# Performance work log

Measured on AMD Instinct MI355X. Metric: run time of the kernel, lower is better.

Reference implementation:

```python
import jax, jax.numpy as jnp
import numpy as np

D_MODEL = 512
N_HEADS = 8
D_K = D_MODEL // N_HEADS  # 64
MAX_LEN = 5000


def _positional_encoding(d_model, max_len):
    pe = np.zeros((max_len, d_model), dtype=np.float32)
    position = np.arange(max_len, dtype=np.float32)[:, None]
    div_term = np.exp(np.arange(0, d_model, 2, dtype=np.float32) * (-np.log(10000.0) / d_model))
    pe[:, 0::2] = np.sin(position * div_term)
    pe[:, 1::2] = np.cos(position * div_term)
    return jnp.asarray(pe)


def _layer_norm(x, gamma, beta, eps):
    mu = jnp.mean(x, axis=-1, keepdims=True)
    var = jnp.mean(jnp.square(x - mu), axis=-1, keepdims=True)
    return (x - mu) * jax.lax.rsqrt(var + eps) * gamma + beta


def setup_inputs() -> dict:
    key = jax.random.key(0)
    ks = jax.random.split(key, 5)
    s = 1.0 / np.sqrt(D_MODEL)
    return {
        "x": jax.random.normal(ks[0], (4, 2048, D_MODEL), dtype=jnp.float32),
        "ln1_g": jnp.ones((D_MODEL,), jnp.float32),
        "ln1_b": jnp.zeros((D_MODEL,), jnp.float32),
        "wq": jax.random.normal(ks[1], (D_MODEL, D_MODEL), jnp.float32) * s,
        "wk": jax.random.normal(ks[2], (D_MODEL, D_MODEL), jnp.float32) * s,
        "wv": jax.random.normal(ks[3], (D_MODEL, D_MODEL), jnp.float32) * s,
        "wfc": jax.random.normal(ks[4], (D_MODEL, D_MODEL), jnp.float32) * s,
        "ln2_g": jnp.ones((D_MODEL,), jnp.float32),
        "ln2_b": jnp.zeros((D_MODEL,), jnp.float32),
    }


def reference(x, ln1_g, ln1_b, wq, wk, wv, wfc, ln2_g, ln2_b):
    B, T, D = x.shape
    residual0 = x
    # outer pre-norm (nn.LayerNorm default eps=1e-5)
    h = _layer_norm(x, ln1_g, ln1_b, 1e-5)
    # sinusoidal positional encoding
    h = h + _positional_encoding(D_MODEL, MAX_LEN)[:T]
    residual1 = h
    # projections -> [B, H, T, d]
    q = (h @ wq).reshape(B, T, N_HEADS, D_K).transpose(0, 2, 1, 3)
    k = (h @ wk).reshape(B, T, N_HEADS, D_K).transpose(0, 2, 1, 3)
    v = (h @ wv).reshape(B, T, N_HEADS, D_K).transpose(0, 2, 1, 3)
    scale = 1.0 / np.sqrt(D_K).astype(np.float32)
    attn = jnp.einsum("bhqd,bhkd->bhqk", q * scale, k)
    causal = jnp.tril(jnp.ones((T, T), dtype=bool))  # subsequent mask
    attn = jnp.where(causal, attn, jnp.float32(-1e9))
    attn = jax.nn.softmax(attn, axis=-1)
    o = jnp.einsum("bhqk,bhkd->bhqd", attn, v)
    o = o.transpose(0, 2, 1, 3).reshape(B, T, D)
    o = o @ wfc
    # inner post-attention residual + LayerNorm (eps=1e-6)
    h2 = _layer_norm(o + residual1, ln2_g, ln2_b, 1e-6)
    return h2 + residual0
```

## Files before the change

### kernel.cpp

```cpp
#include <hip/hip_runtime.h>
#include <hip/hip_bf16.h>

#define B_ 4
#define T_ 2048
#define D_ 512

typedef __attribute__((ext_vector_type(8))) short short8;
typedef __attribute__((ext_vector_type(4))) short short4v;
typedef __attribute__((ext_vector_type(4))) float float4v;
typedef unsigned short bf16_t;

__device__ __forceinline__ bf16_t f2bf(float f) {
  unsigned int u = __builtin_bit_cast(unsigned int, f);
  unsigned int r = (u + 0x7fffu + ((u >> 16) & 1u)) >> 16;
  return (bf16_t)r;
}
__device__ __forceinline__ float bf2f(bf16_t b) {
  unsigned int u = ((unsigned int)b) << 16;
  return __builtin_bit_cast(float, u);
}

__device__ __forceinline__ float fast_exp2(float x) {
#if __has_builtin(__builtin_amdgcn_exp2f)
  return __builtin_amdgcn_exp2f(x);
#else
  float r;
  asm("v_exp_f32 %0, %1" : "=v"(r) : "v"(x));
  return r;
#endif
}

__device__ __forceinline__ unsigned cvt_pk_bf16(float lo, float hi) {
  unsigned r;
  asm("v_cvt_pk_bf16_f32 %0, %1, %2" : "=v"(r) : "v"(lo), "v"(hi));
  return r;
}

__device__ __forceinline__ float waveReduceSum(float v) {
#pragma unroll
  for (int m = 32; m >= 1; m >>= 1) v += __shfl_xor(v, m, 64);
  return v;
}

__device__ __forceinline__ void gld16(const bf16_t* g, bf16_t* l) {
  __builtin_amdgcn_global_load_lds(
      (const __attribute__((address_space(1))) void*)g,
      (__attribute__((address_space(3))) void*)l, 16, 0, 0);
}

__global__ __launch_bounds__(256) void pre_kernel(
    const float* __restrict__ x, const float* __restrict__ g,
    const float* __restrict__ bb,
    const float* __restrict__ wq, const float* __restrict__ wk,
    const float* __restrict__ wv, const float* __restrict__ wfc,
    bf16_t* __restrict__ h_bf16,
    bf16_t* __restrict__ wqkvT, bf16_t* __restrict__ wfcT) {
  if (blockIdx.x >= 2048) {
    __shared__ float tl[64][65];
    int bid = blockIdx.x - 2048;
    const float* src;
    float scl;
    int n0, k0;
    bf16_t* dst;
    if (bid < 192) {
      n0 = (bid >> 3) * 64;
      k0 = (bid & 7) * 64;
      int m = n0 >> 9;
      src = (m == 0) ? wq : ((m == 1) ? wk : wv);
      scl = (m == 0) ? 1.4426950408889634f : ((m == 1) ? 0.125f : 1.0f);
      dst = wqkvT;
    } else {
      int local = bid - 192;
      n0 = (local >> 3) * 64;
      k0 = (local & 7) * 64;
      src = wfc;
      scl = 1.0f;
      dst = wfcT;
    }
    int c0 = n0 & 511;
    int jl = threadIdx.x & 63, bi = threadIdx.x >> 6;
#pragma unroll
    for (int it = 0; it < 16; ++it) {
      int i = it * 4 + bi;
      tl[jl][i] = src[(size_t)(k0 + i) * 512 + c0 + jl] * scl;
    }
    __syncthreads();
    int i2 = (threadIdx.x & 31) * 2, jb = threadIdx.x >> 5;
#pragma unroll
    for (int it = 0; it < 8; ++it) {
      int j = it * 8 + jb;
      unsigned pk = cvt_pk_bf16(tl[j][i2], tl[j][i2 + 1]);
      *(unsigned*)(dst + (size_t)(n0 + j) * 512 + k0 + i2) = pk;
    }
    return;
  }
  int wave = threadIdx.x >> 6, lane = threadIdx.x & 63;
  int row = blockIdx.x * 4 + wave;
  int pos = row & (T_ - 1);
  const float* xr = x + (size_t)row * D_;
  int c0 = lane * 8;
  float v[8];
  float4 a = *(const float4*)(xr + c0);
  float4 b4 = *(const float4*)(xr + c0 + 4);
  v[0]=a.x; v[1]=a.y; v[2]=a.z; v[3]=a.w;
  v[4]=b4.x; v[5]=b4.y; v[6]=b4.z; v[7]=b4.w;
  float s = 0.f;
#pragma unroll
  for (int j = 0; j < 8; ++j) s += v[j];
  s = waveReduceSum(s);
  float mu = s * (1.f / 512.f);
  float q = 0.f;
#pragma unroll
  for (int j = 0; j < 8; ++j) { float d = v[j] - mu; q += d * d; }
  q = waveReduceSum(q);
  float rstd = rsqrtf(q * (1.f / 512.f) + 1e-5f);
  bf16_t* hb = h_bf16 + (size_t)row * D_;
  float fpos = (float)pos;
#pragma unroll
  for (int jp = 0; jp < 4; ++jp) {
    int col = c0 + jp * 2;
    float dt = fast_exp2((float)col * (-13.287712379549449f / 512.0f));
    float ang = fpos * dt;
    float hn0 = (v[2 * jp] - mu) * rstd * g[col] + bb[col] + __sinf(ang);
    float hn1 = (v[2 * jp + 1] - mu) * rstd * g[col + 1] + bb[col + 1] + __cosf(ang);
    hb[col] = f2bf(hn0);
    hb[col + 1] = f2bf(hn1);
  }
}

template <typename EPI>
__device__ __forceinline__ void gemm_body(const bf16_t* __restrict__ A,
                                          const bf16_t* __restrict__ Bt,
                                          int m0, int n0, bf16_t* As, bf16_t* Bs,
                                          EPI epi) {
  const int tid = threadIdx.x;
  const int w = tid >> 6, lane = tid & 63;
  const int ln = lane & 15, quad = lane >> 4;
  const int wy = w >> 1, wx = w & 1;
  const int sw = ln & 7;

  float4v acc[4][4];
  float4v z = {0.f, 0.f, 0.f, 0.f};
#pragma unroll
  for (int i = 0; i < 4; ++i)
#pragma unroll
    for (int j = 0; j < 4; ++j) acc[i][j] = z;

  for (int k0 = 0; k0 < 512; k0 += 64) {
#pragma unroll
    for (int i = 0; i < 4; ++i) {
      int cbase = w * 256 + i * 64;
      int chunk = cbase + lane;
      int row = chunk >> 3;
      int lb = (chunk & 7) ^ (row & 7);
      gld16(A + (size_t)(m0 + row) * 512 + k0 + lb * 8, As + cbase * 8);
      gld16(Bt + (size_t)(n0 + row) * 512 + k0 + lb * 8, Bs + cbase * 8);
    }
    __syncthreads();
#pragma unroll
    for (int c = 0; c < 2; ++c) {
      short8 af[4], bf[4];
#pragma unroll
      for (int mt = 0; mt < 4; ++mt)
        af[mt] = *(const short8*)(As + (wy * 64 + mt * 16 + ln) * 64 + (((c * 4 + quad) ^ sw)) * 8);
#pragma unroll
      for (int nt = 0; nt < 4; ++nt)
        bf[nt] = *(const short8*)(Bs + (wx * 64 + nt * 16 + ln) * 64 + (((c * 4 + quad) ^ sw)) * 8);
#pragma unroll
      for (int mt = 0; mt < 4; ++mt)
#pragma unroll
        for (int nt = 0; nt < 4; ++nt)
          acc[mt][nt] = __builtin_amdgcn_mfma_f32_16x16x32_bf16(af[mt], bf[nt], acc[mt][nt], 0, 0, 0);
    }
    __syncthreads();
  }
#pragma unroll
  for (int mt = 0; mt < 4; ++mt)
#pragma unroll
    for (int r = 0; r < 4; ++r) {
      int row = m0 + wy * 64 + mt * 16 + quad * 4 + r;
#pragma unroll
      for (int nt = 0; nt < 4; ++nt) {
        int col = n0 + wx * 64 + nt * 16 + ln;
        epi(row, col, acc[mt][nt][r]);
      }
    }
}

template <typename EPI>
__device__ __forceinline__ void gemm_body_64x128(const bf16_t* __restrict__ A,
                                                 const bf16_t* __restrict__ Bt,
                                                 int m0, int n0, bf16_t* As, bf16_t* Bs,
                                                 EPI epi) {
  const int tid = threadIdx.x;
  const int w = tid >> 6, lane = tid & 63;
  const int ln = lane & 15, quad = lane >> 4;
  const int wy = w >> 1, wx = w & 1;
  const int sw = ln & 7;

  float4v acc[2][4];
  float4v z = {0.f, 0.f, 0.f, 0.f};
#pragma unroll
  for (int i = 0; i < 2; ++i)
#pragma unroll
    for (int j = 0; j < 4; ++j) acc[i][j] = z;

  for (int k0 = 0; k0 < 512; k0 += 64) {
#pragma unroll
    for (int i = 0; i < 2; ++i) {
      int cbase = i * 256 + w * 64;
      int chunk = cbase + lane;
      int row = chunk >> 3;
      int lb = (chunk & 7) ^ (row & 7);
      gld16(A + (size_t)(m0 + row) * 512 + k0 + lb * 8, As + cbase * 8);
    }
#pragma unroll
    for (int i = 0; i < 4; ++i) {
      int cbase = i * 256 + w * 64;
      int chunk = cbase + lane;
      int row = chunk >> 3;
      int lb = (chunk & 7) ^ (row & 7);
      gld16(Bt + (size_t)(n0 + row) * 512 + k0 + lb * 8, Bs + cbase * 8);
    }
    __syncthreads();
#pragma unroll
    for (int c = 0; c < 2; ++c) {
      short8 af[2], bf[4];
#pragma unroll
      for (int mt = 0; mt < 2; ++mt)
        af[mt] = *(const short8*)(As + (wy * 32 + mt * 16 + ln) * 64 + (((c * 4 + quad) ^ sw)) * 8);
#pragma unroll
      for (int nt = 0; nt < 4; ++nt)
        bf[nt] = *(const short8*)(Bs + (wx * 64 + nt * 16 + ln) * 64 + (((c * 4 + quad) ^ sw)) * 8);
#pragma unroll
      for (int mt = 0; mt < 2; ++mt)
#pragma unroll
        for (int nt = 0; nt < 4; ++nt)
          acc[mt][nt] = __builtin_amdgcn_mfma_f32_16x16x32_bf16(af[mt], bf[nt], acc[mt][nt], 0, 0, 0);
    }
    __syncthreads();
  }
#pragma unroll
  for (int mt = 0; mt < 2; ++mt)
#pragma unroll
    for (int r = 0; r < 4; ++r) {
      int row = m0 + wy * 32 + mt * 16 + quad * 4 + r;
#pragma unroll
      for (int nt = 0; nt < 4; ++nt) {
        int col = n0 + wx * 64 + nt * 16 + ln;
        epi(row, col, acc[mt][nt][r]);
      }
    }
}

__global__ __launch_bounds__(256) void gemm_qkvt_kernel(
    const bf16_t* __restrict__ h_bf, const bf16_t* __restrict__ wqkvT,
    bf16_t* __restrict__ qk, bf16_t* __restrict__ vT) {
  __shared__ __align__(16) bf16_t As[128 * 64];
  __shared__ __align__(16) bf16_t Bs[128 * 64];
  int bx = blockIdx.x;
  if (bx < 512) {
    int m0 = (bx >> 3) * 128, n0 = (bx & 7) * 128;
    gemm_body(h_bf, wqkvT, m0, n0, As, Bs,
              [&](int row, int col, float v) { qk[(size_t)row * 1024 + col] = f2bf(v); });
  } else {
    int local = bx - 512;
    int m0 = (local >> 6) * 128, n0 = (local & 63) * 128;
    gemm_body(wqkvT + 1024 * 512, h_bf, m0, n0, As, Bs,
              [&](int row, int col, float v) { vT[(size_t)row * 8192 + col] = f2bf(v); });
  }
}

__global__ __launch_bounds__(256) void gemm_out_kernel(
    const bf16_t* __restrict__ attn, const bf16_t* __restrict__ wfcT,
    const bf16_t* __restrict__ h_bf, bf16_t* __restrict__ o2r) {
  __shared__ __align__(16) bf16_t As[64 * 64];
  __shared__ __align__(16) bf16_t Bs[128 * 64];
  int bx = blockIdx.x;
  int m0 = (bx >> 2) * 64, n0 = (bx & 3) * 128;
  gemm_body_64x128(attn, wfcT, m0, n0, As, Bs, [&](int row, int col, float v) {
    size_t o = (size_t)row * 512 + col;
    o2r[o] = f2bf(v + bf2f(h_bf[o]));
  });
}

__global__ __launch_bounds__(256) void attn_kernel(const bf16_t* __restrict__ qk,
                                                   const bf16_t* __restrict__ vT,
                                                   bf16_t* __restrict__ out) {
  __shared__ __align__(16) bf16_t Ks[2][64 * 64];
  __shared__ __align__(16) bf16_t Vs[2][64 * 64];
  const int bx = blockIdx.x;
  const int qt = 31 - (bx >> 5);
  const int bh = bx & 31;
  const int b = bh >> 3, h = bh & 7;
  const int tid = threadIdx.x;
  const int w = tid >> 6, lane = tid & 63;
  const int ln = lane & 15, quad = lane >> 4;
  const int sw = ln & 7;

  short8 qf0, qf1;
  {
    size_t qrow = ((size_t)b * T_ + qt * 64 + w * 16 + ln) * 1024 + h * 64;
    qf0 = *(const short8*)(qk + qrow + quad * 8);
    qf1 = *(const short8*)(qk + qrow + 32 + quad * 8);
  }
  float4v z = {0.f, 0.f, 0.f, 0.f};
  float4v oacc[4];
#pragma unroll
  for (int i = 0; i < 4; ++i) oacc[i] = z;
  float m_s = -1e30f, l_s = 0.f;

  const bf16_t* kbase = qk + (size_t)b * T_ * 1024 + 512 + h * 64;
  const bf16_t* vbase = vT + (size_t)(h * 64) * 8192 + (size_t)b * T_;

  const int cb0 = w * 128, cb1 = w * 128 + 64;
  const int ch0 = cb0 + lane, ch1 = cb1 + lane;
  const int r0 = ch0 >> 3, r1 = ch1 >> 3;
  const int lb0 = (ch0 & 7) ^ (r0 & 7), lb1 = (ch1 & 7) ^ (r1 & 7);
  const bf16_t* kg0 = kbase + (size_t)r0 * 1024 + lb0 * 8;
  const bf16_t* kg1 = kbase + (size_t)r1 * 1024 + lb1 * 8;
  const bf16_t* vg0 = vbase + (size_t)r0 * 8192 + lb0 * 8;
  const bf16_t* vg1 = vbase + (size_t)r1 * 8192 + lb1 * 8;

  auto stage2 = [&](int buf) {
    gld16(kg0, Ks[buf] + cb0 * 8);
    gld16(kg1, Ks[buf] + cb1 * 8);
    gld16(vg0, Vs[buf] + cb0 * 8);
    gld16(vg1, Vs[buf] + cb1 * 8);
    kg0 += 64 * 1024; kg1 += 64 * 1024;
    vg0 += 64;        vg1 += 64;
  };

  auto compute = [&](const bf16_t* Kc, const bf16_t* Vc, bool mask) {
    float sv[4][4];
#pragma unroll
    for (int mt = 0; mt < 4; ++mt) {
      float4v st = z;
      int row = mt * 16 + ln;
      short8 a0 = *(const short8*)(Kc + row * 64 + ((0 + quad) ^ sw) * 8);
      short8 a1 = *(const short8*)(Kc + row * 64 + ((4 + quad) ^ sw) * 8);
      st = __builtin_amdgcn_mfma_f32_16x16x32_bf16(a0, qf0, st, 0, 0, 0);
      st = __builtin_amdgcn_mfma_f32_16x16x32_bf16(a1, qf1, st, 0, 0, 0);
#pragma unroll
      for (int r = 0; r < 4; ++r) {
        float v = st[r];
        if (mask) {
          int kloc = mt * 16 + quad * 4 + r;
          if (kloc > w * 16 + ln) v = -1e30f;
        }
        sv[mt][r] = v;
      }
    }
    float mx = sv[0][0];
#pragma unroll
    for (int mt = 0; mt < 4; ++mt)
#pragma unroll
      for (int r = 0; r < 4; ++r) mx = fmaxf(mx, sv[mt][r]);
    mx = fmaxf(mx, __shfl_xor(mx, 16, 64));
    mx = fmaxf(mx, __shfl_xor(mx, 32, 64));
    if (!__all(mx <= m_s + 8.0f)) {
      float mn = fmaxf(m_s, mx);
      float alpha = fast_exp2(m_s - mn);
      m_s = mn;
      l_s *= alpha;
#pragma unroll
      for (int dt = 0; dt < 4; ++dt)
#pragma unroll
        for (int r = 0; r < 4; ++r) oacc[dt][r] *= alpha;
    }
    float rs = 0.f;
#pragma unroll
    for (int mt = 0; mt < 4; ++mt)
#pragma unroll
      for (int r = 0; r < 4; ++r) {
        float p = fast_exp2(sv[mt][r] - m_s);
        sv[mt][r] = p;
        rs += p;
      }
    rs += __shfl_xor(rs, 16, 64);
    rs += __shfl_xor(rs, 32, 64);
    l_s += rs;
    short4v pf[4];
#pragma unroll
    for (int mt = 0; mt < 4; ++mt) {
      uint2 pp;
      pp.x = cvt_pk_bf16(sv[mt][0], sv[mt][1]);
      pp.y = cvt_pk_bf16(sv[mt][2], sv[mt][3]);
      pf[mt] = __builtin_bit_cast(short4v, pp);
    }
#pragma unroll
    for (int dt = 0; dt < 4; ++dt) {
      int row = dt * 16 + ln;
#pragma unroll
      for (int mt = 0; mt < 4; ++mt) {
        short4v av = *(const short4v*)(Vc + row * 64 + ((2 * mt + (quad >> 1)) ^ sw) * 8 + (quad & 1) * 4);
        oacc[dt] = __builtin_amdgcn_mfma_f32_16x16x16bf16_1k(av, pf[mt], oacc[dt], 0, 0, 0);
      }
    }
  };

  stage2(0);
  __syncthreads();
  for (int kt = 0; kt < qt; ++kt) {
    int cur = kt & 1;
    stage2(cur ^ 1);
    compute(Ks[cur], Vs[cur], false);
    __syncthreads();
  }
  compute(Ks[qt & 1], Vs[qt & 1], true);

  float inv = 1.0f / l_s;
  size_t obase = ((size_t)b * T_ + qt * 64 + w * 16 + ln) * 512 + h * 64;
#pragma unroll
  for (int dt = 0; dt < 4; ++dt) {
    short4v o4;
#pragma unroll
    for (int r = 0; r < 4; ++r) o4[r] = (short)f2bf(oacc[dt][r] * inv);
    *(short4v*)(out + obase + dt * 16 + quad * 4) = o4;
  }
}

__global__ __launch_bounds__(256) void ln2_kernel(
    const bf16_t* __restrict__ o2r, const float* __restrict__ x,
    const float* __restrict__ g, const float* __restrict__ bb,
    float* __restrict__ out) {
  int wave = threadIdx.x >> 6, lane = threadIdx.x & 63;
  int row = blockIdx.x * 4 + wave;
  size_t ro = (size_t)row * D_;
  int c0 = lane * 8;
  short8 ov = *(const short8*)(o2r + ro + c0);
  float t[8];
#pragma unroll
  for (int j = 0; j < 8; ++j) t[j] = bf2f((bf16_t)ov[j]);
  float s = 0.f;
#pragma unroll
  for (int j = 0; j < 8; ++j) s += t[j];
  s = waveReduceSum(s);
  float mu = s * (1.f / 512.f);
  float q = 0.f;
#pragma unroll
  for (int j = 0; j < 8; ++j) { float d = t[j] - mu; q += d * d; }
  q = waveReduceSum(q);
  float rstd = rsqrtf(q * (1.f / 512.f) + 1e-6f);
  float4 x0 = *(const float4*)(x + ro + c0);
  float4 x1 = *(const float4*)(x + ro + c0 + 4);
  float xr[8] = {x0.x, x0.y, x0.z, x0.w, x1.x, x1.y, x1.z, x1.w};
  float o[8];
#pragma unroll
  for (int j = 0; j < 8; ++j) {
    int col = c0 + j;
    o[j] = (t[j] - mu) * rstd * g[col] + bb[col] + xr[j];
  }
  float4 w0 = {o[0], o[1], o[2], o[3]};
  float4 w1 = {o[4], o[5], o[6], o[7]};
  *(float4*)(out + ro + c0) = w0;
  *(float4*)(out + ro + c0 + 4) = w1;
}

extern "C" void kernel_launch(void* const* d_in, const int* in_sizes, int n_in,
                              void* d_out, int out_size, void* d_ws, size_t ws_size,
                              hipStream_t stream) {
  const float* x   = (const float*)d_in[0];
  const float* g1  = (const float*)d_in[1];
  const float* b1  = (const float*)d_in[2];
  const float* wq  = (const float*)d_in[3];
  const float* wk  = (const float*)d_in[4];
  const float* wv  = (const float*)d_in[5];
  const float* wfc = (const float*)d_in[6];
  const float* g2  = (const float*)d_in[7];
  const float* b2  = (const float*)d_in[8];
  float* out = (float*)d_out;

  char* ws = (char*)d_ws;
  const size_t O_HBF  = 0;
  const size_t O_WQKV = 8388608;
  const size_t O_WFC  = 9961472;
  const size_t O_QK   = 10485760;
  const size_t O_VT   = 27262976;
  const size_t O_ATTN = 35651584;
  const size_t O_O2R  = 44040192;
  const size_t WS_NEED = 52428800;
  if (ws_size < WS_NEED) return;

  bf16_t* h_bf  = (bf16_t*)(ws + O_HBF);
  bf16_t* wqkvT = (bf16_t*)(ws + O_WQKV);
  bf16_t* wfcT  = (bf16_t*)(ws + O_WFC);
  bf16_t* qk    = (bf16_t*)(ws + O_QK);
  bf16_t* vT    = (bf16_t*)(ws + O_VT);
  bf16_t* attn  = (bf16_t*)(ws + O_ATTN);
  bf16_t* o2r   = (bf16_t*)(ws + O_O2R);

  pre_kernel<<<dim3(2304), dim3(256), 0, stream>>>(x, g1, b1, wq, wk, wv, wfc,
                                                   h_bf, wqkvT, wfcT);
  gemm_qkvt_kernel<<<dim3(768), dim3(256), 0, stream>>>(h_bf, wqkvT, qk, vT);
  attn_kernel<<<dim3(1024), dim3(256), 0, stream>>>(qk, vT, attn);
  gemm_out_kernel<<<dim3(512), dim3(256), 0, stream>>>(attn, wfcT, h_bf, o2r);
  ln2_kernel<<<dim3(2048), dim3(256), 0, stream>>>(o2r, x, g2, b2, out);
}
```

Baseline: 161.8 us.

## Process two query tiles per attention block to reuse staged K/V tiles

Each attention block now handles 128 query rows (two 64-row sub-tiles) instead of 64, so every K/V tile loaded into shared memory feeds MFMAs for both sub-tiles. The grid is halved to 512 blocks, and the first sub-tile stops early with its own mask on its diagonal tile. This cuts global-to-LDS traffic and sync count per query row, but doubles accumulator registers (lower occupancy) and gives fewer, longer blocks with more uneven causal work.

After: 186.7 us. 1.15x slower.

```diff
diff --git a/kernel.cpp b/kernel.cpp
--- a/kernel.cpp
+++ b/kernel.cpp
@@ -290,7 +290,7 @@
   __shared__ __align__(16) bf16_t Ks[2][64 * 64];
   __shared__ __align__(16) bf16_t Vs[2][64 * 64];
   const int bx = blockIdx.x;
-  const int qt = 31 - (bx >> 5);
+  const int t = 15 - (bx >> 5);
   const int bh = bx & 31;
   const int b = bh >> 3, h = bh & 7;
   const int tid = threadIdx.x;
@@ -298,17 +298,22 @@
   const int ln = lane & 15, quad = lane >> 4;
   const int sw = ln & 7;
 
-  short8 qf0, qf1;
-  {
-    size_t qrow = ((size_t)b * T_ + qt * 64 + w * 16 + ln) * 1024 + h * 64;
-    qf0 = *(const short8*)(qk + qrow + quad * 8);
-    qf1 = *(const short8*)(qk + qrow + 32 + quad * 8);
+  const int Nt = 2 * t + 2;
+
+  short8 qf[2][2];
+#pragma unroll
+  for (int s = 0; s < 2; ++s) {
+    size_t qrow = ((size_t)b * T_ + t * 128 + s * 64 + w * 16 + ln) * 1024 + h * 64;
+    qf[s][0] = *(const short8*)(qk + qrow + quad * 8);
+    qf[s][1] = *(const short8*)(qk + qrow + 32 + quad * 8);
   }
   float4v z = {0.f, 0.f, 0.f, 0.f};
-  float4v oacc[4];
-#pragma unroll
-  for (int i = 0; i < 4; ++i) oacc[i] = z;
-  float m_s = -1e30f, l_s = 0.f;
+  float4v oacc[2][4];
+#pragma unroll
+  for (int s = 0; s < 2; ++s)
+#pragma unroll
+    for (int i = 0; i < 4; ++i) oacc[s][i] = z;
+  float m_s[2] = {-1e30f, -1e30f}, l_s[2] = {0.f, 0.f};
 
   const bf16_t* kbase = qk + (size_t)b * T_ * 1024 + 512 + h * 64;
   const bf16_t* vbase = vT + (size_t)(h * 64) * 8192 + (size_t)b * T_;
@@ -331,56 +336,35 @@
     vg0 += 64;        vg1 += 64;
   };
 
-  auto compute = [&](const bf16_t* Kc, const bf16_t* Vc, bool mask) {
-    float sv[4][4];
-#pragma unroll
-    for (int mt = 0; mt < 4; ++mt) {
-      float4v st = z;
-      int row = mt * 16 + ln;
-      short8 a0 = *(const short8*)(Kc + row * 64 + ((0 + quad) ^ sw) * 8);
-      short8 a1 = *(const short8*)(Kc + row * 64 + ((4 + quad) ^ sw) * 8);
-      st = __builtin_amdgcn_mfma_f32_16x16x32_bf16(a0, qf0, st, 0, 0, 0);
-      st = __builtin_amdgcn_mfma_f32_16x16x32_bf16(a1, qf1, st, 0, 0, 0);
-#pragma unroll
-      for (int r = 0; r < 4; ++r) {
-        float v = st[r];
-        if (mask) {
-          int kloc = mt * 16 + quad * 4 + r;
-          if (kloc > w * 16 + ln) v = -1e30f;
-        }
-        sv[mt][r] = v;
-      }
-    }
-    float mx = sv[0][0];
+  auto softmax = [&](float sv[4][4], float& ms, float& ls, float4v* oa, short4v* pf) {
+    float mxa[4];
 #pragma unroll
     for (int mt = 0; mt < 4; ++mt)
-#pragma unroll
-      for (int r = 0; r < 4; ++r) mx = fmaxf(mx, sv[mt][r]);
+      mxa[mt] = fmaxf(fmaxf(sv[mt][0], sv[mt][1]), fmaxf(sv[mt][2], sv[mt][3]));
+    float mx = fmaxf(fmaxf(mxa[0], mxa[1]), fmaxf(mxa[2], mxa[3]));
     mx = fmaxf(mx, __shfl_xor(mx, 16, 64));
     mx = fmaxf(mx, __shfl_xor(mx, 32, 64));
-    if (!__all(mx <= m_s + 8.0f)) {
-      float mn = fmaxf(m_s, mx);
-      float alpha = fast_exp2(m_s - mn);
-      m_s = mn;
-      l_s *= alpha;
+    if (!__all(mx <= ms + 8.0f)) {
+      float mn = fmaxf(ms, mx);
+      float alpha = fast_exp2(ms - mn);
+      ms = mn;
+      ls *= alpha;
 #pragma unroll
       for (int dt = 0; dt < 4; ++dt)
 #pragma unroll
-        for (int r = 0; r < 4; ++r) oacc[dt][r] *= alpha;
-    }
-    float rs = 0.f;
-#pragma unroll
-    for (int mt = 0; mt < 4; ++mt)
-#pragma unroll
-      for (int r = 0; r < 4; ++r) {
-        float p = fast_exp2(sv[mt][r] - m_s);
-        sv[mt][r] = p;
-        rs += p;
-      }
+        for (int r = 0; r < 4; ++r) oa[dt][r] *= alpha;
+    }
+    float rsa[4];
+#pragma unroll
+    for (int mt = 0; mt < 4; ++mt) {
+#pragma unroll
+      for (int r = 0; r < 4; ++r) sv[mt][r] = fast_exp2(sv[mt][r] - ms);
+      rsa[mt] = (sv[mt][0] + sv[mt][1]) + (sv[mt][2] + sv[mt][3]);
+    }
+    float rs = (rsa[0] + rsa[1]) + (rsa[2] + rsa[3]);
     rs += __shfl_xor(rs, 16, 64);
     rs += __shfl_xor(rs, 32, 64);
-    l_s += rs;
-    short4v pf[4];
+    ls += rs;
 #pragma unroll
     for (int mt = 0; mt < 4; ++mt) {
       uint2 pp;
@@ -388,35 +372,79 @@
       pp.y = cvt_pk_bf16(sv[mt][2], sv[mt][3]);
       pf[mt] = __builtin_bit_cast(short4v, pp);
     }
+  };
+
+  auto compute = [&](const bf16_t* Kc, const bf16_t* Vc,
+                     bool act0, bool mask0, bool mask1) {
+    float sv0[4][4], sv1[4][4];
+#pragma unroll
+    for (int mt = 0; mt < 4; ++mt) {
+      int row = mt * 16 + ln;
+      short8 a0 = *(const short8*)(Kc + row * 64 + ((0 + quad) ^ sw) * 8);
+      short8 a1 = *(const short8*)(Kc + row * 64 + ((4 + quad) ^ sw) * 8);
+      float4v st1 = z;
+      st1 = __builtin_amdgcn_mfma_f32_16x16x32_bf16(a0, qf[1][0], st1, 0, 0, 0);
+      st1 = __builtin_amdgcn_mfma_f32_16x16x32_bf16(a1, qf[1][1], st1, 0, 0, 0);
+      if (act0) {
+        float4v st0 = z;
+        st0 = __builtin_amdgcn_mfma_f32_16x16x32_bf16(a0, qf[0][0], st0, 0, 0, 0);
+        st0 = __builtin_amdgcn_mfma_f32_16x16x32_bf16(a1, qf[0][1], st0, 0, 0, 0);
+#pragma unroll
+        for (int r = 0; r < 4; ++r) {
+          float v = st0[r];
+          if (mask0) {
+            int kloc = mt * 16 + quad * 4 + r;
+            if (kloc > w * 16 + ln) v = -1e30f;
+          }
+          sv0[mt][r] = v;
+        }
+      }
+#pragma unroll
+      for (int r = 0; r < 4; ++r) {
+        float v = st1[r];
+        if (mask1) {
+          int kloc = mt * 16 + quad * 4 + r;
+          if (kloc > w * 16 + ln) v = -1e30f;
+        }
+        sv1[mt][r] = v;
+      }
+    }
+    short4v pf0[4], pf1[4];
+    if (act0) softmax(sv0, m_s[0], l_s[0], oacc[0], pf0);
+    softmax(sv1, m_s[1], l_s[1], oacc[1], pf1);
 #pragma unroll
     for (int dt = 0; dt < 4; ++dt) {
       int row = dt * 16 + ln;
 #pragma unroll
       for (int mt = 0; mt < 4; ++mt) {
         short4v av = *(const short4v*)(Vc + row * 64 + ((2 * mt + (quad >> 1)) ^ sw) * 8 + (quad & 1) * 4);
-        oacc[dt] = __builtin_amdgcn_mfma_f32_16x16x16bf16_1k(av, pf[mt], oacc[dt], 0, 0, 0);
+        if (act0)
+          oacc[0][dt] = __builtin_amdgcn_mfma_f32_16x16x16bf16_1k(av, pf0[mt], oacc[0][dt], 0, 0, 0);
+        oacc[1][dt] = __builtin_amdgcn_mfma_f32_16x16x16bf16_1k(av, pf1[mt], oacc[1][dt], 0, 0, 0);
       }
     }
   };
 
   stage2(0);
   __syncthreads();
-  for (int kt = 0; kt < qt; ++kt) {
-    int cur = kt & 1;
-    stage2(cur ^ 1);
-    compute(Ks[cur], Vs[cur], false);
-    __syncthreads();
-  }
-  compute(Ks[qt & 1], Vs[qt & 1], true);
-
-  float inv = 1.0f / l_s;
-  size_t obase = ((size_t)b * T_ + qt * 64 + w * 16 + ln) * 512 + h * 64;
-#pragma unroll
-  for (int dt = 0; dt < 4; ++dt) {
-    short4v o4;
-#pragma unroll
-    for (int r = 0; r < 4; ++r) o4[r] = (short)f2bf(oacc[dt][r] * inv);
-    *(short4v*)(out + obase + dt * 16 + quad * 4) = o4;
+  for (int i = 0; i < Nt; ++i) {
+    int cur = i & 1;
+    if (i + 1 < Nt) stage2(cur ^ 1);
+    compute(Ks[cur], Vs[cur], i <= 2 * t, i == 2 * t, i == 2 * t + 1);
+    if (i + 1 < Nt) __syncthreads();
+  }
+
+#pragma unroll
+  for (int s = 0; s < 2; ++s) {
+    float inv = 1.0f / l_s[s];
+    size_t obase = ((size_t)b * T_ + t * 128 + s * 64 + w * 16 + ln) * 512 + h * 64;
+#pragma unroll
+    for (int dt = 0; dt < 4; ++dt) {
+      short4v o4;
+#pragma unroll
+      for (int r = 0; r < 4; ++r) o4[r] = (short)f2bf(oacc[s][dt][r] * inv);
+      *(short4v*)(out + obase + dt * 16 + quad * 4) = o4;
+    }
   }
 }
 
@@ -493,7 +521,7 @@
   pre_kernel<<<dim3(2304), dim3(256), 0, stream>>>(x, g1, b1, wq, wk, wv, wfc,
                                                    h_bf, wqkvT, wfcT);
   gemm_qkvt_kernel<<<dim3(768), dim3(256), 0, stream>>>(h_bf, wqkvT, qk, vT);
-  attn_kernel<<<dim3(1024), dim3(256), 0, stream>>>(qk, vT, attn);
+  attn_kernel<<<dim3(512), dim3(256), 0, stream>>>(qk, vT, attn);
   gemm_out_kernel<<<dim3(512), dim3(256), 0, stream>>>(attn, wfcT, h_bf, o2r);
   ln2_kernel<<<dim3(2048), dim3(256), 0, stream>>>(o2r, x, g2, b2, out);
 }
```
